# Performance work log

Hardware: AMD Instinct MI355X
Metric: run time of the kernel (lower is better)

The kernel has to match this reference:

```python
import jax, jax.numpy as jnp
import numpy as np

EPS = 1e-5
SIGMA = 1.0

def _conv(x, w, stride):
    return jax.lax.conv_general_dilated(
        x, w, window_strides=(stride, stride),
        padding=[(w.shape[2] // 2, w.shape[2] // 2), (w.shape[3] // 2, w.shape[3] // 2)],
        dimension_numbers=('NCHW', 'OIHW', 'NCHW'))

def _bn(x, gamma, beta, mean, var):
    # inference-mode batchnorm over channel dim (NCHW)
    inv = gamma / jnp.sqrt(var + EPS)
    return x * inv[None, :, None, None] + (beta - mean * inv)[None, :, None, None]

def setup_inputs() -> dict:
    key = jax.random.key(0)
    ks = jax.random.split(key, 8)
    B, M, H, W, K = 8, 128, 64, 64, 6
    x = jax.random.normal(ks[0], (B, M, H, W), jnp.float32)
    cf = jax.random.normal(ks[1], (B, M, H, W), jnp.float32)
    w1 = jax.random.normal(ks[2], (M // 2, M, 3, 3), jnp.float32) * 0.05
    w2 = jax.random.normal(ks[3], (M // 4, M // 2, 3, 3), jnp.float32) * 0.05
    w3 = jax.random.normal(ks[4], (K, M // 4, 1, 1), jnp.float32) * 0.05
    def bn_params(k, c):
        k1, k2 = jax.random.split(k)
        return (jnp.ones((c,), jnp.float32),
                jnp.zeros((c,), jnp.float32),
                jax.random.normal(k1, (c,), jnp.float32) * 0.1,
                jnp.abs(jax.random.normal(k2, (c,), jnp.float32)) * 0.1 + 1.0)
    g1, b1, m1, v1 = bn_params(ks[5], M // 2)
    g2, b2, m2, v2 = bn_params(ks[6], M // 4)
    g3, b3, m3, v3 = bn_params(ks[7], K)
    return dict(x=x, center_features=cf, w1=w1, g1=g1, b1=b1, m1=m1, v1=v1,
                w2=w2, g2=g2, b2=b2, m2=m2, v2=v2,
                w3=w3, g3=g3, b3=b3, m3=m3, v3=v3)

def reference(x, center_features, w1, g1, b1, m1, v1, w2, g2, b2, m2, v2, w3, g3, b3, m3, v3):
    # center branch: conv-bn-relu x2 (stride 2) + 1x1 conv-bn, then spatial mean
    c = jax.nn.relu(_bn(_conv(center_features, w1, 2), g1, b1, m1, v1))
    c = jax.nn.relu(_bn(_conv(c, w2, 2), g2, b2, m2, v2))
    c = _bn(_conv(c, w3, 1), g3, b3, m3, v3)
    centers = c.reshape(c.shape[0], c.shape[1], -1).mean(axis=2)  # [B, K]

    B, C, H, W = x.shape
    K = centers.shape[-1]
    xf = x.reshape(B, C, H * W, 1)                      # [B,C,HW,1]
    cb = centers[:, None, None, :]                      # [B,1,1,K]
    dist = (xf - cb) ** 2                               # [B,C,HW,K]
    phi_soft = jax.nn.softmax(-SIGMA * dist, axis=-1)
    qsoft = jnp.sum(phi_soft * cb, axis=-1).reshape(B, C, H, W)
    symbols = jnp.argmin(dist, axis=-1)                 # [B,C,HW] (== argmax of hard softmax)
    qhard = centers[jnp.arange(B)[:, None, None], symbols].reshape(B, C, H, W)
    qbar = qsoft + jax.lax.stop_gradient(qhard - qsoft)
    return qbar, qsoft, qhard, symbols.reshape(B, C, H, W), centers
```

## Files before the change

kernel.cpp:

```cpp
#include <hip/hip_runtime.h>
#include <math.h>

#define BN_EPS 1e-5
#define SIGMA 1.0f

__global__ __launch_bounds__(256, 4) void conv1_partial_kernel(
    const float* __restrict__ in, const float* __restrict__ w1,
    float* __restrict__ part)
{
    __shared__ double wlds[1152];

    int bid = blockIdx.x;
    int oht = bid & 1;
    int b   = (bid >> 1) & 7;
    int isp = (bid >> 4) & 7;
    int ocg = bid >> 7;

    int tid = threadIdx.x;
    int ow  = tid & 31;
    int ohp = tid >> 5;
    int oh0 = oht * 16 + ohp * 2;
    int ih0 = 2 * oh0 - 1;
    int iw0 = 2 * ow - 1;

    for (int i = tid; i < 1152; i += 256) {
        int j  = i & 7;
        int t  = i >> 3;
        int k  = t % 9;
        int ic = t / 9;
        wlds[i] = (double)w1[((ocg * 8 + j) * 128 + isp * 16 + ic) * 9 + k];
    }
    __syncthreads();

    double acc0[8], acc1[8];
    #pragma unroll
    for (int j = 0; j < 8; ++j) { acc0[j] = 0.0; acc1[j] = 0.0; }

    bool rowok[5], colok[3];
    #pragma unroll
    for (int t = 0; t < 5; ++t) rowok[t] = (ih0 + t) >= 0;
    #pragma unroll
    for (int t = 0; t < 3; ++t) colok[t] = (iw0 + t) >= 0;

    const float* base0 = in + ((size_t)(b * 128 + isp * 16) * 64 + ih0) * 64 + iw0;

    float cur[15];
    #pragma unroll
    for (int t = 0; t < 5; ++t)
        #pragma unroll
        for (int kw = 0; kw < 3; ++kw)
            cur[t * 3 + kw] = (rowok[t] && colok[kw]) ? base0[t * 64 + kw] : 0.f;

    for (int ic = 0; ic < 16; ++ic) {
        float nxt[15];
        if (ic + 1 < 16) {
            const float* basen = base0 + (size_t)(ic + 1) * 4096;
            #pragma unroll
            for (int t = 0; t < 5; ++t)
                #pragma unroll
                for (int kw = 0; kw < 3; ++kw)
                    nxt[t * 3 + kw] = (rowok[t] && colok[kw]) ? basen[t * 64 + kw] : 0.f;
        }
        double xv[15];
        #pragma unroll
        for (int i = 0; i < 15; ++i) xv[i] = (double)cur[i];

        const double* wk = &wlds[ic * 72];
        #pragma unroll
        for (int k = 0; k < 9; ++k) {
            int kh = k / 3, kw = k % 3;
            double2 wa = *(const double2*)&wk[k * 8 + 0];
            double2 wb = *(const double2*)&wk[k * 8 + 2];
            double2 wc = *(const double2*)&wk[k * 8 + 4];
            double2 wd = *(const double2*)&wk[k * 8 + 6];
            double x0 = xv[kh * 3 + kw];
            double x1 = xv[(kh + 2) * 3 + kw];
            acc0[0] = fma(x0, wa.x, acc0[0]);  acc1[0] = fma(x1, wa.x, acc1[0]);
            acc0[1] = fma(x0, wa.y, acc0[1]);  acc1[1] = fma(x1, wa.y, acc1[1]);
            acc0[2] = fma(x0, wb.x, acc0[2]);  acc1[2] = fma(x1, wb.x, acc1[2]);
            acc0[3] = fma(x0, wb.y, acc0[3]);  acc1[3] = fma(x1, wb.y, acc1[3]);
            acc0[4] = fma(x0, wc.x, acc0[4]);  acc1[4] = fma(x1, wc.x, acc1[4]);
            acc0[5] = fma(x0, wc.y, acc0[5]);  acc1[5] = fma(x1, wc.y, acc1[5]);
            acc0[6] = fma(x0, wd.x, acc0[6]);  acc1[6] = fma(x1, wd.x, acc1[6]);
            acc0[7] = fma(x0, wd.y, acc0[7]);  acc1[7] = fma(x1, wd.y, acc1[7]);
        }
        #pragma unroll
        for (int i = 0; i < 15; ++i) cur[i] = nxt[i];
    }

    #pragma unroll
    for (int j = 0; j < 8; ++j) {
        int idx0 = ((b * 64 + ocg * 8 + j) * 32 + oh0) * 32 + ow;
        part[isp * 524288 + idx0]      = (float)acc0[j];
        part[isp * 524288 + idx0 + 32] = (float)acc1[j];
    }
}

__global__ __launch_bounds__(256) void conv1_combine_kernel(
    const float* __restrict__ part,
    const float* __restrict__ g, const float* __restrict__ be,
    const float* __restrict__ mn, const float* __restrict__ vr,
    float* __restrict__ y1)
{
    int idx = blockIdx.x * 256 + threadIdx.x;
    int oc = (idx >> 10) & 63;
    double s = 0.0;
    #pragma unroll
    for (int p = 0; p < 8; ++p) s += (double)part[idx + p * 524288];
    double inv = (double)g[oc] / sqrt((double)vr[oc] + BN_EPS);
    double o = s * inv + ((double)be[oc] - (double)mn[oc] * inv);
    y1[idx] = fmaxf((float)o, 0.f);
}

__global__ __launch_bounds__(256) void conv2_partial_kernel(
    const float* __restrict__ y1, const float* __restrict__ w,
    float* __restrict__ part)
{
    __shared__ float tin[4][33][36];
    __shared__ float twt[4][9][8];

    int bid = blockIdx.x;
    int ocg = bid & 3;
    int b   = (bid >> 2) & 7;
    int isp = bid >> 5;

    int tid = threadIdx.x;
    int ow  = tid & 15;
    int oh  = tid >> 4;

    const float* inb = y1 + (size_t)(b * 64 + isp * 4) * 1024;

    for (int lin = tid; lin < 4 * 33 * 34; lin += 256) {
        int c   = lin % 34;
        int t2  = lin / 34;
        int rr  = t2 % 33;
        int icc = t2 / 33;
        int ih  = rr - 1;
        int iw  = c - 1;
        float v = 0.f;
        if ((unsigned)ih < 32u && (unsigned)iw < 32u)
            v = inb[(icc * 32 + ih) * 32 + iw];
        tin[icc][rr][c] = v;
    }
    for (int i = tid; i < 288; i += 256) {
        int j   = i & 7;
        int k   = (i >> 3) % 9;
        int icc = i / 72;
        twt[icc][k][j] = w[(ocg * 8 + j) * 576 + (isp * 4 + icc) * 9 + k];
    }
    __syncthreads();

    double acc[8];
    #pragma unroll
    for (int j = 0; j < 8; ++j) acc[j] = 0.0;

    for (int icc = 0; icc < 4; ++icc) {
        double xv[9];
        #pragma unroll
        for (int kh = 0; kh < 3; ++kh)
            #pragma unroll
            for (int kw = 0; kw < 3; ++kw)
                xv[kh * 3 + kw] = (double)tin[icc][2 * oh + kh][2 * ow + kw];
        #pragma unroll
        for (int k = 0; k < 9; ++k) {
            float4 wa = *(const float4*)&twt[icc][k][0];
            float4 wb = *(const float4*)&twt[icc][k][4];
            acc[0] = fma(xv[k], (double)wa.x, acc[0]);
            acc[1] = fma(xv[k], (double)wa.y, acc[1]);
            acc[2] = fma(xv[k], (double)wa.z, acc[2]);
            acc[3] = fma(xv[k], (double)wa.w, acc[3]);
            acc[4] = fma(xv[k], (double)wb.x, acc[4]);
            acc[5] = fma(xv[k], (double)wb.y, acc[5]);
            acc[6] = fma(xv[k], (double)wb.z, acc[6]);
            acc[7] = fma(xv[k], (double)wb.w, acc[7]);
        }
    }
    int obase = ((b * 32 + ocg * 8) * 16 + oh) * 16 + ow;
    #pragma unroll
    for (int j = 0; j < 8; ++j)
        part[isp * 65536 + obase + j * 256] = (float)acc[j];
}

__global__ __launch_bounds__(256) void conv2_combine_ybar_kernel(
    const float* __restrict__ part,
    const float* __restrict__ g, const float* __restrict__ be,
    const float* __restrict__ mn, const float* __restrict__ vr,
    double* __restrict__ ybar)
{
    __shared__ double sm[4];
    int j  = blockIdx.x;
    int oc = j & 31;
    int t  = threadIdx.x;
    int idx = j * 256 + t;
    double s = 0.0;
    #pragma unroll
    for (int p = 0; p < 16; ++p) s += (double)part[idx + p * 65536];
    double inv = (double)g[oc] / sqrt((double)vr[oc] + BN_EPS);
    double o = s * inv + ((double)be[oc] - (double)mn[oc] * inv);
    double v = fmax(o, 0.0);
    #pragma unroll
    for (int off = 32; off > 0; off >>= 1) v += __shfl_down(v, off, 64);
    if ((t & 63) == 0) sm[t >> 6] = v;
    __syncthreads();
    if (t == 0) ybar[j] = (sm[0] + sm[1] + sm[2] + sm[3]) * (1.0 / 256.0);
}

__global__ __launch_bounds__(64) void centers_kernel(
    const double* __restrict__ ybar, const float* __restrict__ w3,
    const float* __restrict__ g, const float* __restrict__ be,
    const float* __restrict__ mn, const float* __restrict__ vr,
    double* __restrict__ cen_ws, float* __restrict__ cen_out)
{
    int t = threadIdx.x;
    if (t < 48) {
        int b = t / 6;
        int k = t % 6;
        double acc = 0.0;
        for (int ic = 0; ic < 32; ++ic) acc = fma((double)w3[k * 32 + ic], ybar[b * 32 + ic], acc);
        double inv = (double)g[k] / sqrt((double)vr[k] + BN_EPS);
        double c = acc * inv + ((double)be[k] - (double)mn[k] * inv);
        cen_ws[t]  = c;
        cen_out[t] = (float)c;
    }
}

__global__ __launch_bounds__(256) void quant_kernel(
    const float* __restrict__ x, const double* __restrict__ centers,
    float* __restrict__ qbar, float* __restrict__ qsoft,
    float* __restrict__ qhard, float* __restrict__ sym)
{
    int vid = blockIdx.x * 256 + threadIdx.x;
    int b = vid >> 17;

    double c[6];
    float cf[6];
    #pragma unroll
    for (int k = 0; k < 6; ++k) { c[k] = centers[b * 6 + k]; cf[k] = (float)c[k]; }

    float4 xv = ((const float4*)x)[vid];
    float xs[4] = {xv.x, xv.y, xv.z, xv.w};
    float r_bar[4], r_soft[4], r_hard[4], r_sym[4];

    #pragma unroll
    for (int i = 0; i < 4; ++i) {
        double xx = (double)xs[i];
        double d[6];
        double dmin = 1e300;
        int amin = 0;
        #pragma unroll
        for (int k = 0; k < 6; ++k) {
            double t = xx - c[k];
            d[k] = t * t;
            if (d[k] < dmin) { dmin = d[k]; amin = k; }
        }
        float se = 0.f, sw = 0.f;
        #pragma unroll
        for (int k = 0; k < 6; ++k) {
            float e = __expf(SIGMA * (float)(dmin - d[k]));
            se += e;
            sw += e * cf[k];
        }
        float qs = sw / se;
        float qh = cf[amin];
        r_soft[i] = qs;
        r_hard[i] = qh;
        r_bar[i]  = qh;
        r_sym[i]  = (float)amin;
    }

    ((float4*)qbar)[vid]  = make_float4(r_bar[0],  r_bar[1],  r_bar[2],  r_bar[3]);
    ((float4*)qsoft)[vid] = make_float4(r_soft[0], r_soft[1], r_soft[2], r_soft[3]);
    ((float4*)qhard)[vid] = make_float4(r_hard[0], r_hard[1], r_hard[2], r_hard[3]);
    ((float4*)sym)[vid]   = make_float4(r_sym[0],  r_sym[1],  r_sym[2],  r_sym[3]);
}

extern "C" void kernel_launch(void* const* d_in, const int* in_sizes, int n_in,
                              void* d_out, int out_size, void* d_ws, size_t ws_size,
                              hipStream_t stream) {
    const float* x  = (const float*)d_in[0];
    const float* cf = (const float*)d_in[1];
    const float* w1 = (const float*)d_in[2];
    const float* g1 = (const float*)d_in[3];
    const float* b1 = (const float*)d_in[4];
    const float* m1 = (const float*)d_in[5];
    const float* v1 = (const float*)d_in[6];
    const float* w2 = (const float*)d_in[7];
    const float* g2 = (const float*)d_in[8];
    const float* b2 = (const float*)d_in[9];
    const float* m2 = (const float*)d_in[10];
    const float* v2 = (const float*)d_in[11];
    const float* w3 = (const float*)d_in[12];
    const float* g3 = (const float*)d_in[13];
    const float* b3 = (const float*)d_in[14];
    const float* m3 = (const float*)d_in[15];
    const float* v3 = (const float*)d_in[16];

    const int NELEM = 8 * 128 * 64 * 64;
    float* out   = (float*)d_out;
    float* qbar  = out;
    float* qsoft = out + (size_t)NELEM;
    float* qhard = out + (size_t)2 * NELEM;
    float* sym   = out + (size_t)3 * NELEM;
    float* cen_o = out + (size_t)4 * NELEM;

    char* ws = (char*)d_ws;
    float*  part1 = (float*)(ws);
    float*  y1    = (float*)(ws + 16777216);
    float*  part2 = (float*)(ws + 18874368);
    double* yb    = (double*)(ws + 23068672);
    double* cen   = (double*)(ws + 23070720);

    conv1_partial_kernel<<<1024, 256, 0, stream>>>(cf, w1, part1);
    conv1_combine_kernel<<<2048, 256, 0, stream>>>(part1, g1, b1, m1, v1, y1);
    conv2_partial_kernel<<<512, 256, 0, stream>>>(y1, w2, part2);
    conv2_combine_ybar_kernel<<<256, 256, 0, stream>>>(part2, g2, b2, m2, v2, yb);
    centers_kernel<<<1, 64, 0, stream>>>(yb, w3, g3, b3, m3, v3, cen, cen_o);
    quant_kernel<<<NELEM / 4 / 256, 256, 0, stream>>>(x, cen, qbar, qsoft, qhard, sym);
}
```

Measured before the change: 185.9 us.

## Fuse conv1 split-K reduction into conv2 loader and prestage weights as doubles

Removes the conv1_combine kernel. The conv2 partial kernel now sums the eight conv1 partial buffers, applies BN1 and ReLU while loading its input tile, which saves the y1 write and read and one launch. Conv1 weights are converted to double once by a small pre-kernel into a blocked layout, and conv1 reads them straight from global memory instead of staging them in LDS. The risk is that conv1's inner loop now issues global double2 loads instead of LDS reads. Conv2 also repeats the 8-way partial sum for halo elements that neighbouring blocks share.

```diff
diff --git a/kernel.cpp b/kernel.cpp
--- a/kernel.cpp
+++ b/kernel.cpp
@@ -4,12 +4,26 @@
 #define BN_EPS 1e-5
 #define SIGMA 1.0f
 
+__global__ __launch_bounds__(256) void w1_to_f64_kernel(
+    const float* __restrict__ w1, double* __restrict__ w1d)
+{
+    int i = blockIdx.x * 256 + threadIdx.x;
+    if (i >= 73728) return;
+    int j   = i & 7;
+    int t   = i >> 3;
+    int k   = t % 9;
+    int t2  = t / 9;
+    int ic  = t2 & 15;
+    int t3  = t2 >> 4;
+    int isp = t3 & 7;
+    int ocg = t3 >> 3;
+    w1d[i] = (double)w1[((ocg * 8 + j) * 128 + isp * 16 + ic) * 9 + k];
+}
+
 __global__ __launch_bounds__(256, 4) void conv1_partial_kernel(
-    const float* __restrict__ in, const float* __restrict__ w1,
+    const float* __restrict__ in, const double* __restrict__ w1d,
     float* __restrict__ part)
 {
-    __shared__ double wlds[1152];
-
     int bid = blockIdx.x;
     int oht = bid & 1;
     int b   = (bid >> 1) & 7;
@@ -23,14 +37,7 @@
     int ih0 = 2 * oh0 - 1;
     int iw0 = 2 * ow - 1;
 
-    for (int i = tid; i < 1152; i += 256) {
-        int j  = i & 7;
-        int t  = i >> 3;
-        int k  = t % 9;
-        int ic = t / 9;
-        wlds[i] = (double)w1[((ocg * 8 + j) * 128 + isp * 16 + ic) * 9 + k];
-    }
-    __syncthreads();
+    const double* wb = w1d + (size_t)(ocg * 8 + isp) * 1152;
 
     double acc0[8], acc1[8];
     #pragma unroll
@@ -65,24 +72,24 @@
         #pragma unroll
         for (int i = 0; i < 15; ++i) xv[i] = (double)cur[i];
 
-        const double* wk = &wlds[ic * 72];
+        const double* wk = wb + ic * 72;
         #pragma unroll
         for (int k = 0; k < 9; ++k) {
             int kh = k / 3, kw = k % 3;
             double2 wa = *(const double2*)&wk[k * 8 + 0];
-            double2 wb = *(const double2*)&wk[k * 8 + 2];
+            double2 wb2 = *(const double2*)&wk[k * 8 + 2];
             double2 wc = *(const double2*)&wk[k * 8 + 4];
             double2 wd = *(const double2*)&wk[k * 8 + 6];
             double x0 = xv[kh * 3 + kw];
             double x1 = xv[(kh + 2) * 3 + kw];
-            acc0[0] = fma(x0, wa.x, acc0[0]);  acc1[0] = fma(x1, wa.x, acc1[0]);
-            acc0[1] = fma(x0, wa.y, acc0[1]);  acc1[1] = fma(x1, wa.y, acc1[1]);
-            acc0[2] = fma(x0, wb.x, acc0[2]);  acc1[2] = fma(x1, wb.x, acc1[2]);
-            acc0[3] = fma(x0, wb.y, acc0[3]);  acc1[3] = fma(x1, wb.y, acc1[3]);
-            acc0[4] = fma(x0, wc.x, acc0[4]);  acc1[4] = fma(x1, wc.x, acc1[4]);
-            acc0[5] = fma(x0, wc.y, acc0[5]);  acc1[5] = fma(x1, wc.y, acc1[5]);
-            acc0[6] = fma(x0, wd.x, acc0[6]);  acc1[6] = fma(x1, wd.x, acc1[6]);
-            acc0[7] = fma(x0, wd.y, acc0[7]);  acc1[7] = fma(x1, wd.y, acc1[7]);
+            acc0[0] = fma(x0, wa.x, acc0[0]);   acc1[0] = fma(x1, wa.x, acc1[0]);
+            acc0[1] = fma(x0, wa.y, acc0[1]);   acc1[1] = fma(x1, wa.y, acc1[1]);
+            acc0[2] = fma(x0, wb2.x, acc0[2]);  acc1[2] = fma(x1, wb2.x, acc1[2]);
+            acc0[3] = fma(x0, wb2.y, acc0[3]);  acc1[3] = fma(x1, wb2.y, acc1[3]);
+            acc0[4] = fma(x0, wc.x, acc0[4]);   acc1[4] = fma(x1, wc.x, acc1[4]);
+            acc0[5] = fma(x0, wc.y, acc0[5]);   acc1[5] = fma(x1, wc.y, acc1[5]);
+            acc0[6] = fma(x0, wd.x, acc0[6]);   acc1[6] = fma(x1, wd.x, acc1[6]);
+            acc0[7] = fma(x0, wd.y, acc0[7]);   acc1[7] = fma(x1, wd.y, acc1[7]);
         }
         #pragma unroll
         for (int i = 0; i < 15; ++i) cur[i] = nxt[i];
@@ -96,28 +103,16 @@
     }
 }
 
-__global__ __launch_bounds__(256) void conv1_combine_kernel(
-    const float* __restrict__ part,
-    const float* __restrict__ g, const float* __restrict__ be,
-    const float* __restrict__ mn, const float* __restrict__ vr,
-    float* __restrict__ y1)
-{
-    int idx = blockIdx.x * 256 + threadIdx.x;
-    int oc = (idx >> 10) & 63;
-    double s = 0.0;
-    #pragma unroll
-    for (int p = 0; p < 8; ++p) s += (double)part[idx + p * 524288];
-    double inv = (double)g[oc] / sqrt((double)vr[oc] + BN_EPS);
-    double o = s * inv + ((double)be[oc] - (double)mn[oc] * inv);
-    y1[idx] = fmaxf((float)o, 0.f);
-}
-
 __global__ __launch_bounds__(256) void conv2_partial_kernel(
-    const float* __restrict__ y1, const float* __restrict__ w,
+    const float* __restrict__ part1,
+    const float* __restrict__ g1, const float* __restrict__ be1,
+    const float* __restrict__ mn1, const float* __restrict__ vr1,
+    const float* __restrict__ w,
     float* __restrict__ part)
 {
     __shared__ float tin[4][33][36];
     __shared__ float twt[4][9][8];
+    __shared__ double sinv[4], ssh[4];
 
     int bid = blockIdx.x;
     int ocg = bid & 3;
@@ -128,7 +123,13 @@
     int ow  = tid & 15;
     int oh  = tid >> 4;
 
-    const float* inb = y1 + (size_t)(b * 64 + isp * 4) * 1024;
+    if (tid < 4) {
+        int ch = isp * 4 + tid;
+        double inv = (double)g1[ch] / sqrt((double)vr1[ch] + BN_EPS);
+        sinv[tid] = inv;
+        ssh[tid]  = (double)be1[ch] - (double)mn1[ch] * inv;
+    }
+    __syncthreads();
 
     for (int lin = tid; lin < 4 * 33 * 34; lin += 256) {
         int c   = lin % 34;
@@ -138,8 +139,15 @@
         int ih  = rr - 1;
         int iw  = c - 1;
         float v = 0.f;
-        if ((unsigned)ih < 32u && (unsigned)iw < 32u)
-            v = inb[(icc * 32 + ih) * 32 + iw];
+        if ((unsigned)ih < 32u && (unsigned)iw < 32u) {
+            int ch  = isp * 4 + icc;
+            int idx = ((b * 64 + ch) * 32 + ih) * 32 + iw;
+            double s = 0.0;
+            #pragma unroll
+            for (int p = 0; p < 8; ++p) s += (double)part1[idx + p * 524288];
+            double o = s * sinv[icc] + ssh[icc];
+            v = fmaxf((float)o, 0.f);
+        }
         tin[icc][rr][c] = v;
     }
     for (int i = tid; i < 288; i += 256) {
@@ -305,14 +313,14 @@
 
     char* ws = (char*)d_ws;
     float*  part1 = (float*)(ws);
-    float*  y1    = (float*)(ws + 16777216);
-    float*  part2 = (float*)(ws + 18874368);
-    double* yb    = (double*)(ws + 23068672);
-    double* cen   = (double*)(ws + 23070720);
-
-    conv1_partial_kernel<<<1024, 256, 0, stream>>>(cf, w1, part1);
-    conv1_combine_kernel<<<2048, 256, 0, stream>>>(part1, g1, b1, m1, v1, y1);
-    conv2_partial_kernel<<<512, 256, 0, stream>>>(y1, w2, part2);
+    float*  part2 = (float*)(ws + 16777216);
+    double* yb    = (double*)(ws + 20971520);
+    double* cen   = (double*)(ws + 20973568);
+    double* w1d   = (double*)(ws + 20975616);
+
+    w1_to_f64_kernel<<<288, 256, 0, stream>>>(w1, w1d);
+    conv1_partial_kernel<<<1024, 256, 0, stream>>>(cf, w1d, part1);
+    conv2_partial_kernel<<<512, 256, 0, stream>>>(part1, g1, b1, m1, v1, w2, part2);
     conv2_combine_ybar_kernel<<<256, 256, 0, stream>>>(part2, g2, b2, m2, v2, yb);
     centers_kernel<<<1, 64, 0, stream>>>(yb, w3, g3, b3, m3, v3, cen, cen_o);
     quant_kernel<<<NELEM / 4 / 256, 256, 0, stream>>>(x, cen, qbar, qsoft, qhard, sym);
```

Result: no change. 188.0 us (+1.1%).
